# Kernel optimization log

Hardware: AMD Instinct MI355X
Metric: run time of the kernel (lower is better)

## Reference

```python
import jax, jax.numpy as jnp
import numpy as np

D_MODEL = 1024
N_HEADS = 16
HEAD_DIM = D_MODEL // N_HEADS
SCALE = HEAD_DIM ** -0.5


def setup_inputs() -> dict:
    key = jax.random.key(0)
    ks = jax.random.split(key, 5)
    B, T = 2, 2048
    w_std = D_MODEL ** -0.5  # ~ torch Linear init scale
    return {
        "x": jax.random.normal(ks[0], (B, T, D_MODEL), dtype=jnp.float32),
        "W_q": jax.random.normal(ks[1], (D_MODEL, D_MODEL), dtype=jnp.float32) * w_std,
        "W_k": jax.random.normal(ks[2], (D_MODEL, D_MODEL), dtype=jnp.float32) * w_std,
        "W_v": jax.random.normal(ks[3], (D_MODEL, D_MODEL), dtype=jnp.float32) * w_std,
        "W_o": jax.random.normal(ks[4], (D_MODEL, D_MODEL), dtype=jnp.float32) * w_std,
    }


def reference(x, W_q, W_k, W_v, W_o):
    # torch Linear: y = x @ W.T  (weight stored as (out, in))
    B, T, _ = x.shape

    def split_heads(y):  # (B,T,D) -> (B,H,T,hd)
        return y.reshape(B, T, N_HEADS, HEAD_DIM).transpose(0, 2, 1, 3)

    q = split_heads(x @ W_q.T)
    k = split_heads(x @ W_k.T)
    v = split_heads(x @ W_v.T)

    attn = jnp.einsum("bhqd,bhkd->bhqk", q, k) * SCALE  # (B,H,T,T)
    attn = jax.nn.softmax(attn, axis=-1)
    out = jnp.einsum("bhqk,bhkd->bhqd", attn, v)  # (B,H,T,hd)
    out = out.transpose(0, 2, 1, 3).reshape(B, T, D_MODEL)
    return out @ W_o.T
```

## Files before the change

kernel.cpp:

```cpp
#include <hip/hip_runtime.h>
#include <hip/hip_bf16.h>

#define D_MODEL 1024
#define N_HEADS 16
#define HEAD_DIM 64
#define SEQ 2048
#define BATCH 2

typedef __attribute__((ext_vector_type(8))) short bf16x8;
typedef __attribute__((ext_vector_type(4))) float f32x4;

typedef __attribute__((address_space(3))) unsigned lds_uint;
typedef __attribute__((address_space(1))) const unsigned global_cuint;

__device__ __forceinline__ void async_cp16(const ushort* g, ushort* l) {
  __builtin_amdgcn_global_load_lds((global_cuint*)g, (lds_uint*)l, 16, 0, 0);
}

__device__ __forceinline__ ushort f2b(float f) {
  union { float f; unsigned u; } x; x.f = f;
  unsigned r = x.u + 0x7fffu + ((x.u >> 16) & 1u);
  return (ushort)(r >> 16);
}

__device__ __forceinline__ unsigned pk2(float a, float b) {
  __hip_bfloat162 h = __float22bfloat162_rn(float2{a, b});
  union { __hip_bfloat162 h; unsigned u; } x; x.h = h;
  return x.u;
}

__device__ __forceinline__ float blo(unsigned u) {
  union { unsigned u; float f; } x; x.u = u << 16; return x.f;
}
__device__ __forceinline__ float bhi(unsigned u) {
  union { unsigned u; float f; } x; x.u = u & 0xffff0000u; return x.f;
}

__device__ __forceinline__ int swz64(int row, int colbyte) {
  return row * 64 + ((colbyte ^ ((row & 7) << 4)) >> 1);
}

__global__ __launch_bounds__(256) void cast_all(const float* __restrict__ x,
                                                const float* __restrict__ Wq,
                                                const float* __restrict__ Wk,
                                                const float* __restrict__ Wv,
                                                const float* __restrict__ Wo,
                                                ushort* __restrict__ xb,
                                                ushort* __restrict__ wqkv,
                                                ushort* __restrict__ wob) {
  int idx = blockIdx.x * 256 + threadIdx.x;
  const float* in;
  uint2* out;
  if (idx < (1 << 20)) {
    in = x; out = (uint2*)xb;
  } else {
    int j = idx - (1 << 20);
    int w = j >> 18;
    idx = j & 0x3FFFF;
    switch (w) {
      case 0: in = Wq; out = (uint2*)wqkv; break;
      case 1: in = Wk; out = (uint2*)(wqkv) + (1 << 18); break;
      case 2: in = Wv; out = (uint2*)(wqkv) + (2 << 18); break;
      default: in = Wo; out = (uint2*)wob; break;
    }
  }
  float4 v = ((const float4*)in)[idx];
  uint2 o; o.x = pk2(v.x, v.y); o.y = pk2(v.z, v.w);
  out[idx] = o;
}

__global__ __launch_bounds__(256) void gemm_qkv(const ushort* __restrict__ A,
                                                const ushort* __restrict__ Bw,
                                                ushort* __restrict__ Qh,
                                                ushort* __restrict__ Kh,
                                                ushort* __restrict__ Vth,
                                                float qscale) {
  constexpr int K = 1024;
  const int bm = blockIdx.y * 128;
  const int bn = blockIdx.x * 128;
  const int tid = threadIdx.x;
  const int wave = tid >> 6;
  const int lane = tid & 63;
  const int l16 = lane & 15;
  const int quad = lane >> 4;

  __shared__ ushort As[128 * 64];
  __shared__ ushort Bs[128 * 64];

  const int wm = (wave & 1) * 64;
  const int wn = (wave >> 1) * 64;

  f32x4 acc[4][4];
#pragma unroll
  for (int r = 0; r < 4; ++r)
#pragma unroll
    for (int c = 0; c < 4; ++c) acc[r][c] = (f32x4){0.f, 0.f, 0.f, 0.f};

  const int srow = wave * 8 + (lane >> 3);
  const int scol = (lane & 7) * 8;

  for (int k0 = 0; k0 < K; k0 += 64) {
#pragma unroll
    for (int j = 0; j < 4; ++j) {
      async_cp16(A  + (size_t)(bm + j * 32 + srow) * K + k0 + scol, &As[(j * 32 + wave * 8) * 64]);
      async_cp16(Bw + (size_t)(bn + j * 32 + srow) * K + k0 + scol, &Bs[(j * 32 + wave * 8) * 64]);
    }
    __syncthreads();

    bf16x8 a[2][4], b[2][4];
#pragma unroll
    for (int ks = 0; ks < 2; ++ks)
#pragma unroll
      for (int r = 0; r < 4; ++r) {
        a[ks][r] = *(const bf16x8*)(&As[(wm + r * 16 + l16) * 64 + ks * 32 + quad * 8]);
        b[ks][r] = *(const bf16x8*)(&Bs[(wn + r * 16 + l16) * 64 + ks * 32 + quad * 8]);
      }
#pragma unroll
    for (int ks = 0; ks < 2; ++ks)
#pragma unroll
      for (int r = 0; r < 4; ++r)
#pragma unroll
        for (int c = 0; c < 4; ++c)
          acc[r][c] = __builtin_amdgcn_mfma_f32_16x16x32_bf16(a[ks][r], b[ks][c], acc[r][c], 0, 0, 0);
    __syncthreads();
  }

#pragma unroll
  for (int r = 0; r < 4; ++r) {
#pragma unroll
    for (int c = 0; c < 4; ++c) {
      int ncol = bn + wn + c * 16 + l16;
      int w = ncol >> 10;
      int f = ncol & 1023;
      int h = f >> 6, d = f & 63;
      if (w == 2) {
        int m0 = bm + wm + r * 16 + quad * 4;
        int b = m0 >> 11, t0 = m0 & 2047;
        uint2 pp;
        pp.x = pk2(acc[r][c][0], acc[r][c][1]);
        pp.y = pk2(acc[r][c][2], acc[r][c][3]);
        *(uint2*)(&Vth[((size_t)(b * 1024 + f) << 11) + t0]) = pp;
      } else {
#pragma unroll
        for (int rr = 0; rr < 4; ++rr) {
          float v = acc[r][c][rr];
          int m = bm + wm + r * 16 + quad * 4 + rr;
          int b = m >> 11, t = m & 2047;
          if (w == 0)
            Qh[((size_t)(b * 16 + h) * SEQ + t) * 64 + d] = f2b(v * qscale);
          else
            Kh[((size_t)(b * 16 + h) * SEQ + t) * 64 + d] = f2b(v);
        }
      }
    }
  }
}

__global__ __launch_bounds__(256) void gemm_out(const ushort* __restrict__ A,
                                                const ushort* __restrict__ Bw,
                                                float* __restrict__ out) {
  constexpr int K = 1024;
  const int bm = blockIdx.y * 64;
  const int bn = blockIdx.x * 128;
  const int tid = threadIdx.x;
  const int wave = tid >> 6;
  const int lane = tid & 63;
  const int l16 = lane & 15;
  const int quad = lane >> 4;

  __shared__ ushort As[64 * 64];
  __shared__ ushort Bs[128 * 64];

  const int wm = (wave & 1) * 32;
  const int wn = (wave >> 1) * 64;

  f32x4 acc[2][4];
#pragma unroll
  for (int r = 0; r < 2; ++r)
#pragma unroll
    for (int c = 0; c < 4; ++c) acc[r][c] = (f32x4){0.f, 0.f, 0.f, 0.f};

  const int srow = wave * 8 + (lane >> 3);
  const int scol = (lane & 7) * 8;

  for (int k0 = 0; k0 < K; k0 += 64) {
#pragma unroll
    for (int j = 0; j < 2; ++j)
      async_cp16(A + (size_t)(bm + j * 32 + srow) * K + k0 + scol, &As[(j * 32 + wave * 8) * 64]);
#pragma unroll
    for (int j = 0; j < 4; ++j)
      async_cp16(Bw + (size_t)(bn + j * 32 + srow) * K + k0 + scol, &Bs[(j * 32 + wave * 8) * 64]);
    __syncthreads();

    bf16x8 a[2][2], b[2][4];
#pragma unroll
    for (int ks = 0; ks < 2; ++ks) {
#pragma unroll
      for (int r = 0; r < 2; ++r)
        a[ks][r] = *(const bf16x8*)(&As[(wm + r * 16 + l16) * 64 + ks * 32 + quad * 8]);
#pragma unroll
      for (int c = 0; c < 4; ++c)
        b[ks][c] = *(const bf16x8*)(&Bs[(wn + c * 16 + l16) * 64 + ks * 32 + quad * 8]);
    }
#pragma unroll
    for (int ks = 0; ks < 2; ++ks)
#pragma unroll
      for (int r = 0; r < 2; ++r)
#pragma unroll
        for (int c = 0; c < 4; ++c)
          acc[r][c] = __builtin_amdgcn_mfma_f32_16x16x32_bf16(a[ks][r], b[ks][c], acc[r][c], 0, 0, 0);
    __syncthreads();
  }

#pragma unroll
  for (int r = 0; r < 2; ++r)
#pragma unroll
    for (int c = 0; c < 4; ++c)
#pragma unroll
      for (int rr = 0; rr < 4; ++rr) {
        int m = bm + wm + r * 16 + quad * 4 + rr;
        int n = bn + wn + c * 16 + l16;
        out[(size_t)m * D_MODEL + n] = acc[r][c][rr];
      }
}

__global__ __launch_bounds__(256, 2) void attn_kernel(const ushort* __restrict__ Qh,
                                                      const ushort* __restrict__ Kh,
                                                      const ushort* __restrict__ Vth,
                                                      ushort* __restrict__ O1,
                                                      ushort* __restrict__ O2,
                                                      float* __restrict__ l1,
                                                      float* __restrict__ l2) {
  const int id = blockIdx.x;
  const int stream = id & 63;
  const int qb = id >> 6;
  const int bh = stream >> 1;
  const int half = stream & 1;
  const int q0 = qb * 128;
  ushort* __restrict__ Op = half ? O2 : O1;
  float* __restrict__ lp = half ? l2 : l1;

  const int tid = threadIdx.x;
  const int wave = tid >> 6;
  const int lane = tid & 63;
  const int l16 = lane & 15;
  const int quad = lane >> 4;

  __shared__ ushort KVbuf[2][2][64 * 64];
  __shared__ ushort Pt[64 * 64];

  bf16x8 qf[2][2];
#pragma unroll
  for (int g = 0; g < 2; ++g) {
    const ushort* qp = Qh + ((size_t)bh * SEQ + q0 + wave * 32 + g * 16 + l16) * 64 + quad * 8;
    qf[g][0] = *(const bf16x8*)(qp);
    qf[g][1] = *(const bf16x8*)(qp + 32);
  }

  f32x4 o[2][4];
  float lacc[2] = {0.f, 0.f};
#pragma unroll
  for (int g = 0; g < 2; ++g)
#pragma unroll
    for (int c = 0; c < 4; ++c) o[g][c] = (f32x4){0.f, 0.f, 0.f, 0.f};

  const int chunk = wave * 2;
  const int r8 = lane >> 3;
  const int csw = (((lane & 7) ^ r8) << 3);
  const ushort* kbase = Kh + ((size_t)bh * SEQ + half * 1024) * 64;
  const ushort* vbase = Vth + (size_t)bh * 64 * SEQ + half * 1024;
  const ushort* ksrc = kbase + (size_t)(chunk * 8 + r8) * 64 + csw;
  const ushort* vsrc = vbase + (size_t)(chunk * 8 + r8) * SEQ + csw;

  async_cp16(ksrc,           &KVbuf[0][0][chunk * 512]);
  async_cp16(ksrc + 8 * 64,  &KVbuf[0][0][(chunk + 1) * 512]);
  async_cp16(vsrc,           &KVbuf[0][1][chunk * 512]);
  async_cp16(vsrc + 8 * SEQ, &KVbuf[0][1][(chunk + 1) * 512]);

  constexpr int NIT = 1024 / 64;
  for (int kt = 0; kt < NIT; ++kt) {
    __syncthreads();
    const int buf = kt & 1;
    if (kt + 1 < NIT) {
      const ushort* ks = ksrc + (size_t)(kt + 1) * 64 * 64;
      const ushort* vs = vsrc + (kt + 1) * 64;
      async_cp16(ks,           &KVbuf[buf ^ 1][0][chunk * 512]);
      async_cp16(ks + 8 * 64,  &KVbuf[buf ^ 1][0][(chunk + 1) * 512]);
      async_cp16(vs,           &KVbuf[buf ^ 1][1][chunk * 512]);
      async_cp16(vs + 8 * SEQ, &KVbuf[buf ^ 1][1][(chunk + 1) * 512]);
    }
    const ushort* Kt = KVbuf[buf][0];
    const ushort* Vt = KVbuf[buf][1];
    const int prow = wave * 16 + l16;

    bf16x8 pf[2][2];
#pragma unroll
    for (int g = 0; g < 2; ++g) {
#pragma unroll
      for (int c = 0; c < 4; ++c) {
        bf16x8 ka0 = *(const bf16x8*)(&Kt[swz64(c * 16 + l16, quad * 16)]);
        bf16x8 ka1 = *(const bf16x8*)(&Kt[swz64(c * 16 + l16, 64 + quad * 16)]);
        f32x4 z = (f32x4){0.f, 0.f, 0.f, 0.f};
        z = __builtin_amdgcn_mfma_f32_16x16x32_bf16(ka0, qf[g][0], z, 0, 0, 0);
        z = __builtin_amdgcn_mfma_f32_16x16x32_bf16(ka1, qf[g][1], z, 0, 0, 0);
        float e0 = __builtin_amdgcn_exp2f(z[0]);
        float e1 = __builtin_amdgcn_exp2f(z[1]);
        float e2 = __builtin_amdgcn_exp2f(z[2]);
        float e3 = __builtin_amdgcn_exp2f(z[3]);
        lacc[g] += (e0 + e1) + (e2 + e3);
        uint2 pp;
        pp.x = pk2(e0, e1);
        pp.y = pk2(e2, e3);
        *(uint2*)(&Pt[swz64(prow, c * 32 + quad * 8)]) = pp;
      }
      pf[g][0] = *(const bf16x8*)(&Pt[swz64(prow, quad * 16)]);
      pf[g][1] = *(const bf16x8*)(&Pt[swz64(prow, 64 + quad * 16)]);
    }

#pragma unroll
    for (int c = 0; c < 4; ++c) {
      bf16x8 vb0 = *(const bf16x8*)(&Vt[swz64(c * 16 + l16, quad * 16)]);
      bf16x8 vb1 = *(const bf16x8*)(&Vt[swz64(c * 16 + l16, 64 + quad * 16)]);
#pragma unroll
      for (int g = 0; g < 2; ++g) {
        o[g][c] = __builtin_amdgcn_mfma_f32_16x16x32_bf16(pf[g][0], vb0, o[g][c], 0, 0, 0);
        o[g][c] = __builtin_amdgcn_mfma_f32_16x16x32_bf16(pf[g][1], vb1, o[g][c], 0, 0, 0);
      }
    }
  }

#pragma unroll
  for (int g = 0; g < 2; ++g) {
    lacc[g] += __shfl_xor(lacc[g], 16, 64);
    lacc[g] += __shfl_xor(lacc[g], 32, 64);
    if (quad == 0)
      lp[(size_t)bh * SEQ + q0 + wave * 32 + g * 16 + l16] = lacc[g];
  }

  __syncthreads();
  ushort* Ob = &KVbuf[0][0][0];
#pragma unroll
  for (int g = 0; g < 2; ++g)
#pragma unroll
    for (int r = 0; r < 4; ++r) {
      int row = wave * 32 + g * 16 + quad * 4 + r;
#pragma unroll
      for (int c = 0; c < 4; ++c)
        Ob[row * 64 + c * 16 + l16] = f2b(o[g][c][r]);
    }
  __syncthreads();
  {
    uint4* dst = (uint4*)(Op + ((size_t)bh * SEQ + q0) * 64);
    const uint4* src = (const uint4*)Ob;
#pragma unroll
    for (int i = 0; i < 4; ++i)
      dst[i * 256 + tid] = src[i * 256 + tid];
  }
}

__global__ __launch_bounds__(256) void recombine(const ushort* __restrict__ O1,
                                                 const ushort* __restrict__ O2,
                                                 const float* __restrict__ l1,
                                                 const float* __restrict__ l2,
                                                 ushort* __restrict__ ctx) {
  int idx = blockIdx.x * 256 + threadIdx.x;
  int row = idx >> 3;
  int d8 = idx & 7;
  uint4 a = ((const uint4*)O1)[idx];
  uint4 b = ((const uint4*)O2)[idx];
  float linv = 1.f / (l1[row] + l2[row]);
  uint4 res;
  unsigned* ap = (unsigned*)&a;
  unsigned* bp = (unsigned*)&b;
  unsigned* rp = (unsigned*)&res;
#pragma unroll
  for (int i = 0; i < 4; ++i) {
    float lo = (blo(ap[i]) + blo(bp[i])) * linv;
    float hi = (bhi(ap[i]) + bhi(bp[i])) * linv;
    rp[i] = pk2(lo, hi);
  }
  int bh = row >> 11, t = row & 2047;
  int bb = bh >> 4, h = bh & 15;
  ((uint4*)ctx)[(size_t)(bb * SEQ + t) * 128 + h * 8 + d8] = res;
}

extern "C" void kernel_launch(void* const* d_in, const int* in_sizes, int n_in,
                              void* d_out, int out_size, void* d_ws, size_t ws_size,
                              hipStream_t stream) {
  const float* x  = (const float*)d_in[0];
  const float* Wq = (const float*)d_in[1];
  const float* Wk = (const float*)d_in[2];
  const float* Wv = (const float*)d_in[3];
  const float* Wo = (const float*)d_in[4];
  float* out = (float*)d_out;

  char* ws = (char*)d_ws;
  const size_t MB = 1 << 20;
  ushort* xb   = (ushort*)(ws);
  ushort* wqkv = (ushort*)(ws +  8 * MB);
  ushort* wob  = (ushort*)(ws + 14 * MB);
  ushort* Qh   = (ushort*)(ws + 16 * MB);
  ushort* Kh   = (ushort*)(ws + 24 * MB);
  ushort* Vth  = (ushort*)(ws + 32 * MB);
  ushort* ctx  = (ushort*)(ws + 40 * MB);

  ushort* O1 = (ushort*)d_out;
  ushort* O2 = xb;
  float*  l1 = (float*)wqkv;
  float*  l2 = (float*)(ws + 8 * MB + 256 * 1024);

  cast_all<<<8192, 256, 0, stream>>>(x, Wq, Wk, Wv, Wo, xb, wqkv, wob);

  const float qscale = 0.125f * 1.44269504089f;
  gemm_qkv<<<dim3(3072 / 128, 4096 / 128), 256, 0, stream>>>(xb, wqkv, Qh, Kh, Vth, qscale);

  attn_kernel<<<(SEQ / 128) * BATCH * N_HEADS * 2, 256, 0, stream>>>(
      Qh, Kh, Vth, O1, O2, l1, l2);

  recombine<<<(BATCH * N_HEADS * SEQ * 64 / 8) / 256, 256, 0, stream>>>(O1, O2, l1, l2, ctx);

  gemm_out<<<dim3(1024 / 128, 4096 / 64), 256, 0, stream>>>(ctx, wob, out);
}
```

Measured before the change: 206.5 us.

## Double-buffer LDS tiles and XOR-swizzle columns in QKV and output GEMMs

Both projection GEMMs now hold two LDS buffers per operand and issue the async global-to-LDS copies for the next K tile before computing on the current one, with one barrier per iteration instead of two. The global source column is XOR-swizzled by row so the MFMA fragment reads through swz64 avoid LDS bank conflicts. This is meant to hide global load latency and cut LDS conflict stalls, at the cost of doubled LDS use, which may lower occupancy. It relies on a pre-existing swz64 helper matching the swizzle pattern.

```diff
diff --git a/kernel.cpp b/kernel.cpp
--- a/kernel.cpp
+++ b/kernel.cpp
@@ -84,8 +84,8 @@
   const int l16 = lane & 15;
   const int quad = lane >> 4;
 
-  __shared__ ushort As[128 * 64];
-  __shared__ ushort Bs[128 * 64];
+  __shared__ ushort As[2][128 * 64];
+  __shared__ ushort Bs[2][128 * 64];
 
   const int wm = (wave & 1) * 64;
   const int wn = (wave >> 1) * 64;
@@ -97,23 +97,34 @@
     for (int c = 0; c < 4; ++c) acc[r][c] = (f32x4){0.f, 0.f, 0.f, 0.f};
 
   const int srow = wave * 8 + (lane >> 3);
-  const int scol = (lane & 7) * 8;
-
-  for (int k0 = 0; k0 < K; k0 += 64) {
-#pragma unroll
-    for (int j = 0; j < 4; ++j) {
-      async_cp16(A  + (size_t)(bm + j * 32 + srow) * K + k0 + scol, &As[(j * 32 + wave * 8) * 64]);
-      async_cp16(Bw + (size_t)(bn + j * 32 + srow) * K + k0 + scol, &Bs[(j * 32 + wave * 8) * 64]);
-    }
+  const int csw = (((lane & 7) ^ (lane >> 3)) << 3);
+
+#pragma unroll
+  for (int j = 0; j < 4; ++j) {
+    async_cp16(A  + (size_t)(bm + j * 32 + srow) * K + csw, &As[0][(j * 32 + wave * 8) * 64]);
+    async_cp16(Bw + (size_t)(bn + j * 32 + srow) * K + csw, &Bs[0][(j * 32 + wave * 8) * 64]);
+  }
+
+  constexpr int NIT = K / 64;
+  for (int kt = 0; kt < NIT; ++kt) {
     __syncthreads();
+    const int buf = kt & 1;
+    if (kt + 1 < NIT) {
+      const int k0 = (kt + 1) * 64;
+#pragma unroll
+      for (int j = 0; j < 4; ++j) {
+        async_cp16(A  + (size_t)(bm + j * 32 + srow) * K + k0 + csw, &As[buf ^ 1][(j * 32 + wave * 8) * 64]);
+        async_cp16(Bw + (size_t)(bn + j * 32 + srow) * K + k0 + csw, &Bs[buf ^ 1][(j * 32 + wave * 8) * 64]);
+      }
+    }
 
     bf16x8 a[2][4], b[2][4];
 #pragma unroll
     for (int ks = 0; ks < 2; ++ks)
 #pragma unroll
       for (int r = 0; r < 4; ++r) {
-        a[ks][r] = *(const bf16x8*)(&As[(wm + r * 16 + l16) * 64 + ks * 32 + quad * 8]);
-        b[ks][r] = *(const bf16x8*)(&Bs[(wn + r * 16 + l16) * 64 + ks * 32 + quad * 8]);
+        a[ks][r] = *(const bf16x8*)(&As[buf][swz64(wm + r * 16 + l16, ks * 64 + quad * 16)]);
+        b[ks][r] = *(const bf16x8*)(&Bs[buf][swz64(wn + r * 16 + l16, ks * 64 + quad * 16)]);
       }
 #pragma unroll
     for (int ks = 0; ks < 2; ++ks)
@@ -122,7 +133,6 @@
 #pragma unroll
         for (int c = 0; c < 4; ++c)
           acc[r][c] = __builtin_amdgcn_mfma_f32_16x16x32_bf16(a[ks][r], b[ks][c], acc[r][c], 0, 0, 0);
-    __syncthreads();
   }
 
 #pragma unroll
@@ -168,8 +178,8 @@
   const int l16 = lane & 15;
   const int quad = lane >> 4;
 
-  __shared__ ushort As[64 * 64];
-  __shared__ ushort Bs[128 * 64];
+  __shared__ ushort As[2][64 * 64];
+  __shared__ ushort Bs[2][128 * 64];
 
   const int wm = (wave & 1) * 32;
   const int wn = (wave >> 1) * 64;
@@ -181,26 +191,38 @@
     for (int c = 0; c < 4; ++c) acc[r][c] = (f32x4){0.f, 0.f, 0.f, 0.f};
 
   const int srow = wave * 8 + (lane >> 3);
-  const int scol = (lane & 7) * 8;
-
-  for (int k0 = 0; k0 < K; k0 += 64) {
-#pragma unroll
-    for (int j = 0; j < 2; ++j)
-      async_cp16(A + (size_t)(bm + j * 32 + srow) * K + k0 + scol, &As[(j * 32 + wave * 8) * 64]);
-#pragma unroll
-    for (int j = 0; j < 4; ++j)
-      async_cp16(Bw + (size_t)(bn + j * 32 + srow) * K + k0 + scol, &Bs[(j * 32 + wave * 8) * 64]);
+  const int csw = (((lane & 7) ^ (lane >> 3)) << 3);
+
+#pragma unroll
+  for (int j = 0; j < 2; ++j)
+    async_cp16(A + (size_t)(bm + j * 32 + srow) * K + csw, &As[0][(j * 32 + wave * 8) * 64]);
+#pragma unroll
+  for (int j = 0; j < 4; ++j)
+    async_cp16(Bw + (size_t)(bn + j * 32 + srow) * K + csw, &Bs[0][(j * 32 + wave * 8) * 64]);
+
+  constexpr int NIT = K / 64;
+  for (int kt = 0; kt < NIT; ++kt) {
     __syncthreads();
+    const int buf = kt & 1;
+    if (kt + 1 < NIT) {
+      const int k0 = (kt + 1) * 64;
+#pragma unroll
+      for (int j = 0; j < 2; ++j)
+        async_cp16(A + (size_t)(bm + j * 32 + srow) * K + k0 + csw, &As[buf ^ 1][(j * 32 + wave * 8) * 64]);
+#pragma unroll
+      for (int j = 0; j < 4; ++j)
+        async_cp16(Bw + (size_t)(bn + j * 32 + srow) * K + k0 + csw, &Bs[buf ^ 1][(j * 32 + wave * 8) * 64]);
+    }
 
     bf16x8 a[2][2], b[2][4];
 #pragma unroll
     for (int ks = 0; ks < 2; ++ks) {
 #pragma unroll
       for (int r = 0; r < 2; ++r)
-        a[ks][r] = *(const bf16x8*)(&As[(wm + r * 16 + l16) * 64 + ks * 32 + quad * 8]);
+        a[ks][r] = *(const bf16x8*)(&As[buf][swz64(wm + r * 16 + l16, ks * 64 + quad * 16)]);
 #pragma unroll
       for (int c = 0; c < 4; ++c)
-        b[ks][c] = *(const bf16x8*)(&Bs[(wn + c * 16 + l16) * 64 + ks * 32 + quad * 8]);
+        b[ks][c] = *(const bf16x8*)(&Bs[buf][swz64(wn + c * 16 + l16, ks * 64 + quad * 16)]);
     }
 #pragma unroll
     for (int ks = 0; ks < 2; ++ks)
@@ -209,7 +231,6 @@
 #pragma unroll
         for (int c = 0; c < 4; ++c)
           acc[r][c] = __builtin_amdgcn_mfma_f32_16x16x32_bf16(a[ks][r], b[ks][c], acc[r][c], 0, 0, 0);
-    __syncthreads();
   }
 
 #pragma unroll
```

Result: faster. 198.9 us (-3.7%).
